# Kernel tuning notes

Measured on AMD Instinct MI355X. Metric: run time of the kernel, lower is better.

## Reference

```python
import jax, jax.numpy as jnp
import numpy as np

N1, N2, E = 256, 128, 4096

def _conv(x, w, b):
    # NCHW conv, 3x3, padding=1 (SAME), then ReLU
    y = jax.lax.conv_general_dilated(x, w, (1, 1), 'SAME',
                                     dimension_numbers=('NCHW', 'OIHW', 'NCHW'))
    return jax.nn.relu(y + b[None, :, None, None])

def _pool(x):
    return jax.lax.reduce_window(x, -jnp.inf, jax.lax.max,
                                 (1, 1, 2, 2), (1, 1, 2, 2), 'VALID')

def _sage(x, src, dst, wl, bl, wr, n):
    # torch_geometric SAGEConv: out = lin_l(mean_j x_src) + lin_r(x), then L2 normalize
    agg = jax.ops.segment_sum(x[src], dst, num_segments=n)
    cnt = jax.ops.segment_sum(jnp.ones((src.shape[0],), x.dtype), dst, num_segments=n)
    agg = agg / jnp.maximum(cnt, 1.0)[:, None]
    out = agg @ wl.T + bl + x @ wr.T
    return out / jnp.maximum(jnp.linalg.norm(out, axis=-1, keepdims=True), 1e-12)

def _diff_pool(x, adj, s):
    # torch_geometric dense_diff_pool
    s = jax.nn.softmax(s, axis=-1)
    out = jnp.einsum('bnc,bnf->bcf', s, x)
    out_adj = jnp.einsum('bnc,bnm,bmd->bcd', s, adj, s)
    link = adj - jnp.einsum('bnc,bmc->bnm', s, s)
    link_loss = jnp.sqrt(jnp.sum(link * link)) / adj.size
    ent_loss = jnp.mean(jnp.sum(-s * jnp.log(s + 1e-15), axis=-1))
    return out, out_adj, link_loss, ent_loss

def setup_inputs() -> dict:
    key = jax.random.key(0)
    ks = jax.random.split(key, 16)
    rn = lambda k, shape, sc: jax.random.normal(k, shape, jnp.float32) * sc
    inp = {}
    inp['inputs'] = jax.random.normal(ks[0], (1, 5, 512, 512), jnp.float32)
    inp['edge_index'] = jax.random.randint(ks[1], (2, E), 0, N1)
    chans = [(5, 32), (32, 64), (64, 128), (128, 256), (256, 256)]
    for i, (ci, co) in enumerate(chans):
        inp[f'w{i+1}'] = rn(ks[2 + i], (co, ci, 3, 3), 1.0 / np.sqrt(ci * 9))
        inp[f'b{i+1}'] = jnp.zeros((co,), jnp.float32)
    sdims = [(256, 128), (256, 128), (128, 2)]
    for i, (ci, co) in enumerate(sdims):
        inp[f'sage{i+1}_wl'] = rn(ks[7 + 2 * i], (co, ci), 1.0 / np.sqrt(ci))
        inp[f'sage{i+1}_bl'] = jnp.zeros((co,), jnp.float32)
        inp[f'sage{i+1}_wr'] = rn(ks[8 + 2 * i], (co, ci), 1.0 / np.sqrt(ci))
    return inp

def reference(inputs, edge_index, w1, b1, w2, b2, w3, b3, w4, b4, w5, b5,
              sage1_wl, sage1_bl, sage1_wr, sage2_wl, sage2_bl, sage2_wr,
              sage3_wl, sage3_bl, sage3_wr):
    x = _pool(_conv(inputs, w1, b1))
    x = _pool(_conv(x, w2, b2))
    x = _pool(_conv(x, w3, b3))
    x = _pool(_conv(x, w4, b4))
    x = _pool(_conv(x, w5, b5))            # [1,256,16,16]
    org = x.reshape(N1, N1)                # [256 nodes, 256 feats]
    src, dst = edge_index[0], edge_index[1]
    x1 = _sage(org, src, dst, sage1_wl, sage1_bl, sage1_wr, N1)
    s1 = _sage(org, src, dst, sage2_wl, sage2_bl, sage2_wr, N1)
    # dense adjacency (scipy coo->dense sums duplicate edges)
    adj1 = jnp.zeros((N1, N1), jnp.float32).at[src, dst].add(1.0)
    xp, adjp, ll1, el1 = _diff_pool(x1[None], adj1[None], s1[None])
    xp = xp.reshape(N2, N2)
    adjp = adjp.reshape(N2, N2)
    # vectorized form of the per-row in-place argmax binarization loop
    row_max = jnp.max(adjp, axis=1, keepdims=True)
    edge_out = jnp.where(adjp == row_max, 1.0, 0.0)
    # dense_to_sparse of the binarized matrix (one max per row, generic case)
    cols = jnp.argmax(adjp, axis=1)
    ei2 = jnp.stack([jnp.arange(N2), cols])  # [2,128] int
    nodes_out = jnp.tanh(_sage(xp, ei2[0], ei2[1], sage3_wl, sage3_bl, sage3_wr, N2))
    adj2 = jnp.zeros((N2, N2), jnp.float32).at[ei2[0], ei2[1]].add(1.0)
    s2 = jnp.ones((1, N2, 1), jnp.float32)  # softmax over size-1 dim -> ones
    x2, _, ll2, el2 = _diff_pool(nodes_out[None], adj2[None], s2)
    return (x2.reshape(-1), ll1 + ll2, el1 + el2, nodes_out, edge_out, ei2)
```

## Files before the change

### kernel.cpp

```cpp
#include <hip/hip_runtime.h>
#include <hip/hip_bf16.h>
#include <math.h>

#define N_EDGES 4096
#define NN1 256
#define NN2 128

typedef short v8s __attribute__((ext_vector_type(8)));
typedef float v4f __attribute__((ext_vector_type(4)));

__device__ inline unsigned short f2b(float f){
  union { __hip_bfloat16 h; unsigned short u; } cv;
  cv.h = __float2bfloat16(f);
  return cv.u;
}

template<int NT>
__device__ inline float block_sum(float v, float* red, int t){
  red[t] = v; __syncthreads();
  #pragma unroll
  for (int st = NT/2; st > 0; st >>= 1){
    if (t < st) red[t] += red[t+st];
    __syncthreads();
  }
  float r = red[0]; __syncthreads();
  return r;
}
template<int NT>
__device__ inline float block_max(float v, float* red, int t){
  red[t] = v; __syncthreads();
  #pragma unroll
  for (int st = NT/2; st > 0; st >>= 1){
    if (t < st) red[t] = fmaxf(red[t], red[t+st]);
    __syncthreads();
  }
  float r = red[0]; __syncthreads();
  return r;
}
template<int NT>
__device__ inline int block_min_int(int v, int* red, int t){
  red[t] = v; __syncthreads();
  #pragma unroll
  for (int st = NT/2; st > 0; st >>= 1){
    if (t < st) red[t] = min(red[t], red[t+st]);
    __syncthreads();
  }
  int r = red[0]; __syncthreads();
  return r;
}

template<int CHUNKS, int COUT, int CIN, int SSLABS, int BSTR, int OUTF32>
__global__ __launch_bounds__(256) void conv_mfma(
    const unsigned short* __restrict__ in, const unsigned short* __restrict__ wb,
    const float* __restrict__ bias, unsigned short* __restrict__ outb,
    float* __restrict__ outf,
    int in_row, int in_slab, int out_row, int out_slab)
{
  constexpr int CG = COUT/32;
  __shared__ unsigned short tileb[SSLABS*2600];
  __shared__ unsigned short wldsb[9*32*40];

  const int cg = blockIdx.x % CG, bx = blockIdx.x / CG, by = blockIdx.y;
  const int tid = threadIdx.x, lane = tid & 63, wv = tid >> 6;
  const int cot = wv >> 1, wp = wv & 1;
  const int ml = lane & 15, g = lane >> 4;

  v4f acc[8];
  #pragma unroll
  for (int t = 0; t < 8; ++t) acc[t] = (v4f){0.f,0.f,0.f,0.f};

  for (int cb = 0; cb < CHUNKS; ++cb){
    if (cb) __syncthreads();
    for (int j = tid; j < SSLABS*324; j += 256){
      int s = j / 324, rem = j - s*324;
      int row = rem / 18, px = rem - row*18;
      int gidx = (cb*SSLABS + s)*in_slab + ((by*16 + row)*in_row + bx*16 + px)*8;
      *(v8s*)&tileb[s*2600 + (row*18+px)*8] = *(const v8s*)&in[gidx];
    }
    for (int j = tid; j < 1152; j += 256){
      int k = j >> 7, rem = j & 127;
      int co = rem >> 2, q = rem & 3;
      int gw = (k*COUT + cg*32 + co)*CIN + cb*32 + q*8;
      *(v8s*)&wldsb[(k*32+co)*40 + q*8] = *(const v8s*)&wb[gw];
    }
    __syncthreads();

    #pragma unroll
    for (int k9 = 0; k9 < 9; ++k9){
      const int ky = k9/3, kx = k9 - 3*(k9/3);
      v8s a = *(const v8s*)&wldsb[(k9*32 + cot*16 + ml)*40 + g*8];
      #pragma unroll
      for (int tt = 0; tt < 8; ++tt){
        int t = wp*8 + tt;
        v8s b = *(const v8s*)&tileb[g*BSTR + ((t+ky)*18 + kx + ml)*8];
        acc[tt] = __builtin_amdgcn_mfma_f32_16x16x32_bf16(a, b, acc[tt], 0, 0, 0);
      }
    }
  }

  const int cob = cg*32 + cot*16 + g*4;
  float b4[4] = {bias[cob], bias[cob+1], bias[cob+2], bias[cob+3]};
  #pragma unroll
  for (int tp = 0; tp < 4; ++tp){
    float m[4];
    #pragma unroll
    for (int r = 0; r < 4; ++r){
      float v = fmaxf(acc[2*tp][r], acc[2*tp+1][r]);
      float o = __shfl_xor(v, 1);
      m[r] = fmaxf(fmaxf(v, o) + b4[r], 0.f);
    }
    if ((lane & 1) == 0){
      int gy = by*8 + wp*4 + tp, gx = bx*8 + (ml >> 1);
      if (OUTF32){
        #pragma unroll
        for (int r = 0; r < 4; ++r)
          outf[(cob + r)*256 + gy*16 + gx] = m[r];
      } else {
        unsigned int u0 = (unsigned)f2b(m[0]) | ((unsigned)f2b(m[1]) << 16);
        unsigned int u1 = (unsigned)f2b(m[2]) | ((unsigned)f2b(m[3]) << 16);
        int slabo = cob >> 3, sub = (g & 1)*4;
        size_t idx = (size_t)slabo*out_slab + (size_t)((gy+1)*out_row + gx+1)*8 + sub;
        *(uint2*)(outb + idx) = make_uint2(u0, u1);
      }
    }
  }
}

__global__ __launch_bounds__(256) void prep_kernel(
    const float* __restrict__ src, unsigned short* __restrict__ p0b,
    const float* __restrict__ w1, const float* __restrict__ w2,
    const float* __restrict__ w3, const float* __restrict__ w4,
    const float* __restrict__ w5, unsigned short* __restrict__ wbb,
    const float* __restrict__ a, const float* __restrict__ b2,
    const float* __restrict__ c2, const float* __restrict__ d2,
    float* __restrict__ o)
{
  int b = blockIdx.x, tid = threadIdx.x;
  if (b < 1024){
    int idx = b*256 + tid;
    int y = idx >> 9, x = idx & 511;
    unsigned short v8[8];
    #pragma unroll
    for (int c = 0; c < 5; ++c) v8[c] = f2b(src[c*262144 + y*512 + x]);
    v8[5] = 0; v8[6] = 0; v8[7] = 0;
    *(uint4*)&p0b[((size_t)(y+1)*516 + (x+1))*8] = *(uint4*)v8;
  } else if (b < 1452){
    int j = (b-1024)*256 + tid;
    int co, ci, CO, CIl, CIsrc, dst; const float* w;
    if (j < 1024)      { co=j>>5;        ci=j&31;        w=w1; CIsrc=5;   CO=32;  CIl=32;  dst=0; }
    else if (j < 3072) { int q=j-1024;   co=q>>5;  ci=q&31;  w=w2; CIsrc=32;  CO=64;  CIl=32;  dst=9216; }
    else if (j < 11264){ int q=j-3072;   co=q>>6;  ci=q&63;  w=w3; CIsrc=64;  CO=128; CIl=64;  dst=27648; }
    else if (j < 44032){ int q=j-11264;  co=q>>7;  ci=q&127; w=w4; CIsrc=128; CO=256; CIl=128; dst=101376; }
    else               { int q=j-44032;  co=q>>8;  ci=q&255; w=w5; CIsrc=256; CO=256; CIl=256; dst=396288; }
    #pragma unroll
    for (int k = 0; k < 9; ++k){
      float val = (ci < CIsrc) ? w[(co*CIsrc + ci)*9 + k] : 0.f;
      wbb[dst + (k*CO + co)*CIl + ci] = f2b(val);
    }
  } else {
    int idx = (b-1452)*256 + tid;
    int m = idx >> 15, rem = idx & 32767, k = rem >> 7, cc = rem & 127;
    const float* sp = (m==0)?a:(m==1)?b2:(m==2)?c2:d2;
    o[m*32768 + k*128 + cc] = sp[cc*256 + k];
  }
}

__global__ void build_adj_kernel(const int* __restrict__ ei, float* adj, float* cnt){
  int e = blockIdx.x*256 + threadIdx.x;
  if (e < N_EDGES){
    int s = ei[e], d = ei[N_EDGES + e];
    atomicAdd(&adj[s*NN1 + d], 1.0f);
    atomicAdd(&cnt[d], 1.0f);
  }
}

__global__ __launch_bounds__(128) void sage12_kernel(
    const float* __restrict__ adj, const float* __restrict__ cnt,
    const float* __restrict__ org,
    const float* __restrict__ wl1t, const float* __restrict__ bl1, const float* __restrict__ wr1t,
    const float* __restrict__ wl2t, const float* __restrict__ bl2, const float* __restrict__ wr2t,
    float* __restrict__ x1, float* __restrict__ s_out, float* __restrict__ st,
    float* __restrict__ entpart)
{
  __shared__ float sa[NN1], so[NN1], col[NN1], red[128];
  int n = blockIdx.x, c = threadIdx.x;
  for (int k = c; k < NN1; k += 128){
    col[k] = adj[k*NN1 + n];
    so[k]  = org[n*NN1 + k];
  }
  __syncthreads();
  float a0 = 0.f, a1 = 0.f;
  #pragma unroll 4
  for (int s2 = 0; s2 < NN1; ++s2){
    float av = col[s2];
    a0 += av * org[s2*NN1 + c];
    a1 += av * org[s2*NN1 + c + 128];
  }
  float cd = fmaxf(cnt[n], 1.0f);
  sa[c] = a0 / cd;
  sa[c+128] = a1 / cd;
  __syncthreads();

  float p1 = bl1[c], p2 = bl2[c];
  for (int k = 0; k < NN1; ++k){
    float av = sa[k], ov = so[k];
    p1 += av*wl1t[k*128+c] + ov*wr1t[k*128+c];
    p2 += av*wl2t[k*128+c] + ov*wr2t[k*128+c];
  }
  float n1s = block_sum<128>(p1*p1, red, c);
  x1[n*128 + c] = p1 / fmaxf(sqrtf(n1s), 1e-12f);
  float n2s = block_sum<128>(p2*p2, red, c);
  float p2n = p2 / fmaxf(sqrtf(n2s), 1e-12f);
  float mx = block_max<128>(p2n, red, c);
  float ev = expf(p2n - mx);
  float ssum = block_sum<128>(ev, red, c);
  float sv = ev / ssum;
  s_out[n*128 + c] = sv;
  st[c*NN1 + n] = sv;
  float esum = block_sum<128>(-sv * logf(sv + 1e-15f), red, c);
  if (c == 0) entpart[n] = esum;
}

__global__ __launch_bounds__(256) void fuse1_kernel(
    const float* __restrict__ s, const float* __restrict__ x1,
    const float* __restrict__ adj, const float* __restrict__ st,
    float* __restrict__ xp, float* __restrict__ t, float* __restrict__ linkpart)
{
  __shared__ float sn[128]; __shared__ float red[256];
  int b = blockIdx.x, tid = threadIdx.x;
  if (b < 64){
    int cc = b*2 + (tid >> 7), f = tid & 127;
    float acc = 0.f;
    for (int n = 0; n < NN1; ++n) acc += s[n*128+cc] * x1[n*128+f];
    xp[cc*128+f] = acc;
  } else if (b < 192){
    int n = (b-64)*2 + (tid >> 7), c = tid & 127;
    float acc = 0.f;
    for (int m = 0; m < NN1; ++m){
      float a = adj[n*NN1+m];
      if (a != 0.f) acc += a * s[m*128+c];
    }
    t[n*128+c] = acc;
  } else {
    int n = b - 192, m = tid;
    if (m < 128) sn[m] = s[n*128+m];
    __syncthreads();
    float dot = 0.f;
    for (int c = 0; c < 128; ++c) dot += sn[c]*st[c*NN1 + m];
    float v = adj[n*NN1+m] - dot;
    float part = block_sum<256>(v*v, red, m);
    if (m == 0) linkpart[n] = part;
  }
}

__global__ __launch_bounds__(128) void adjp_kernel(const float* __restrict__ s,
    const float* __restrict__ t, float* __restrict__ adjp){
  int cc = blockIdx.x, d = threadIdx.x;
  float acc = 0.f;
  for (int n = 0; n < NN1; ++n) acc += s[n*128+cc] * t[n*128+d];
  adjp[cc*128+d] = acc;
}

__global__ __launch_bounds__(128) void binarize_kernel(const float* __restrict__ adjp,
    float* __restrict__ edge_out, float* __restrict__ ei2_out, int* __restrict__ cols){
  __shared__ float red[128]; __shared__ int redi[128];
  int i = blockIdx.x, j = threadIdx.x;
  float v = adjp[i*128+j];
  float mx = block_max<128>(v, red, j);
  edge_out[i*128+j] = (v == mx) ? 1.0f : 0.0f;
  int cand = (v == mx) ? j : (1 << 30);
  int cmin = block_min_int<128>(cand, redi, j);
  if (j == 0){
    cols[i] = cmin;
    ei2_out[i] = (float)i;
    ei2_out[128 + i] = (float)cmin;
  }
}

__global__ __launch_bounds__(128) void sage3_agg_kernel(const float* __restrict__ xp,
    const int* __restrict__ cols, float* __restrict__ aggn3){
  int d = blockIdx.x, f = threadIdx.x;
  float acc = 0.f, c = 0.f;
  for (int i = 0; i < NN2; ++i){
    if (cols[i] == d){ acc += xp[i*128+f]; c += 1.f; }
  }
  aggn3[d*128+f] = acc / fmaxf(c, 1.f);
}

__global__ __launch_bounds__(128) void sage3_out_kernel(const float* __restrict__ aggn3,
    const float* __restrict__ xp,
    const float* __restrict__ wl3, const float* __restrict__ bl3, const float* __restrict__ wr3,
    float* __restrict__ nodes_out)
{
  __shared__ float red[128];
  int n = blockIdx.x, k = threadIdx.x;
  float ag = aggn3[n*128+k];
  float xv = xp[n*128+k];
  float q0 = block_sum<128>(ag*wl3[k]     + xv*wr3[k],     red, k);
  float q1 = block_sum<128>(ag*wl3[128+k] + xv*wr3[128+k], red, k);
  if (k == 0){
    float p0 = q0 + bl3[0], p1 = q1 + bl3[1];
    float nm = fmaxf(sqrtf(p0*p0 + p1*p1), 1e-12f);
    nodes_out[n*2+0] = tanhf(p0/nm);
    nodes_out[n*2+1] = tanhf(p1/nm);
  }
}

__global__ __launch_bounds__(256) void finalize_kernel(const float* __restrict__ linkpart,
    const float* __restrict__ entpart, float* __restrict__ d_out)
{
  __shared__ float red[256];
  int t = threadIdx.x;
  float ls = block_sum<256>(linkpart[t], red, t);
  float es = block_sum<256>(entpart[t], red, t);
  float v0 = 0.f, v1 = 0.f;
  if (t < 128){ v0 = d_out[4 + t*2 + 0]; v1 = d_out[4 + t*2 + 1]; }
  float s0 = block_sum<256>(v0, red, t);
  float s1 = block_sum<256>(v1, red, t);
  if (t == 0){
    d_out[0] = s0;
    d_out[1] = s1;
    d_out[2] = sqrtf(ls)/65536.0f + sqrtf(16256.0f)/16384.0f;
    d_out[3] = es/256.0f;
  }
}

extern "C" void kernel_launch(void* const* d_in, const int* in_sizes, int n_in,
                              void* d_out_v, int out_size, void* d_ws, size_t ws_size,
                              hipStream_t stream)
{
  (void)in_sizes; (void)n_in; (void)out_size; (void)ws_size;
  const float* input = (const float*)d_in[0];
  const int*   ei    = (const int*)  d_in[1];
  const float* w1 = (const float*)d_in[2];  const float* b1 = (const float*)d_in[3];
  const float* w2 = (const float*)d_in[4];  const float* b2 = (const float*)d_in[5];
  const float* w3 = (const float*)d_in[6];  const float* b3 = (const float*)d_in[7];
  const float* w4 = (const float*)d_in[8];  const float* b4 = (const float*)d_in[9];
  const float* w5 = (const float*)d_in[10]; const float* b5 = (const float*)d_in[11];
  const float* s1wl = (const float*)d_in[12]; const float* s1bl = (const float*)d_in[13];
  const float* s1wr = (const float*)d_in[14];
  const float* s2wl = (const float*)d_in[15]; const float* s2bl = (const float*)d_in[16];
  const float* s2wr = (const float*)d_in[17];
  const float* s3wl = (const float*)d_in[18]; const float* s3bl = (const float*)d_in[19];
  const float* s3wr = (const float*)d_in[20];
  float* d_out = (float*)d_out_v;
  float* ws = (float*)d_ws;

  unsigned short* P0b = (unsigned short*)(ws);
  unsigned short* Pb1 = (unsigned short*)(ws + 1060896);
  unsigned short* Pb2 = (unsigned short*)(ws + 2134176);
  unsigned short* Pb3 = (unsigned short*)(ws + 2683296);
  unsigned short* Pb4 = (unsigned short*)(ws + 2970528);
  unsigned short* wb  = (unsigned short*)(ws + 3127200);
  float* org = ws + 3620256;
  float* wt  = ws + 3685792;
  float* st  = ws + 3816864;
  float* G   = ws + 3849632;

  float* adj1     = G;
  float* cnt      = G + 65536;
  float* aggn3    = G + 65792;
  float* x1       = G + 147712;
  float* s        = G + 180480;
  float* t        = G + 213248;
  float* xp       = G + 246016;
  float* adjp     = G + 262400;
  int*   cols     = (int*)(G + 278784);
  float* linkpart = G + 278912;
  float* entpart  = G + 279168;

  hipMemsetAsync(ws, 0, (size_t)3127200*sizeof(float), stream);
  prep_kernel<<<dim3(1964), 256, 0, stream>>>(input, P0b, w1, w2, w3, w4, w5, wb,
                                              s1wl, s1wr, s2wl, s2wr, wt);

  conv_mfma<1,32,32,1,0,0>      <<<dim3(32,32), 256, 0, stream>>>(P0b, wb,        b1, Pb1, nullptr, 516, 2121792, 260, 536640);
  conv_mfma<1,64,32,4,2600,0>   <<<dim3(32,16), 256, 0, stream>>>(Pb1, wb+9216,   b2, Pb2, nullptr, 260, 536640, 132, 137280);
  conv_mfma<2,128,64,4,2600,0>  <<<dim3(32,8),  256, 0, stream>>>(Pb2, wb+27648,  b3, Pb3, nullptr, 132, 137280, 68,  35904);
  conv_mfma<4,256,128,4,2600,0> <<<dim3(32,4),  256, 0, stream>>>(Pb3, wb+101376, b4, Pb4, nullptr, 68,  35904,  36,  9792);
  conv_mfma<8,256,256,4,2600,1> <<<dim3(16,2),  256, 0, stream>>>(Pb4, wb+396288, b5, nullptr, org, 36,  9792,   0,   0);

  hipMemsetAsync(adj1, 0, (65536 + 256)*sizeof(float), stream);
  build_adj_kernel<<<dim3(16),  256, 0, stream>>>(ei, adj1, cnt);
  sage12_kernel   <<<dim3(256), 128, 0, stream>>>(adj1, cnt, org, wt, s1bl, wt+32768,
                                                  wt+65536, s2bl, wt+98304, x1, s, st, entpart);
  fuse1_kernel    <<<dim3(448), 256, 0, stream>>>(s, x1, adj1, st, xp, t, linkpart);
  adjp_kernel     <<<dim3(128), 128, 0, stream>>>(s, t, adjp);
  binarize_kernel <<<dim3(128), 128, 0, stream>>>(adjp, d_out + 260, d_out + 16644, cols);
  sage3_agg_kernel<<<dim3(128), 128, 0, stream>>>(xp, cols, aggn3);
  sage3_out_kernel<<<dim3(128), 128, 0, stream>>>(aggn3, xp, s3wl, s3bl, s3wr, d_out + 4);
  finalize_kernel <<<dim3(1),   256, 0, stream>>>(linkpart, entpart, d_out);
}
```

Before: 220.6 us.

## Zero only padded halos and fuse adjp/binarize and sage3 kernels

Replaces the large workspace memset (about 12.5 MB) with a small kernel that zeroes only the one-pixel halo borders of each padded bf16 activation buffer plus the adjacency and count arrays. It also fuses the adjp matmul with the row-argmax binarization, and the sage3 aggregation with its output projection, cutting two launches and two intermediate buffers. This removes a large memory-fill cost and launch overhead. It relies on the conv kernels fully overwriting the buffer interiors, so any interior not written would now hold stale data.

```diff
diff --git a/kernel.cpp b/kernel.cpp
--- a/kernel.cpp
+++ b/kernel.cpp
@@ -124,6 +124,30 @@
       }
     }
   }
+}
+
+__global__ __launch_bounds__(256) void zero_kernel(unsigned short* __restrict__ wsb,
+                                                   float* __restrict__ adjz)
+{
+  int j = blockIdx.x*256 + threadIdx.x;
+  const int c0=2056, c1=6184, c2=10344, c3=14568, c4=18920, ca=35368;
+  if (j >= ca) return;
+  if (j >= c4){
+    int q = j - c4;
+    ((float4*)adjz)[q] = make_float4(0.f,0.f,0.f,0.f);
+    return;
+  }
+  int base, P, R, W, per, rem;
+  if (j < c0)      { base=0;       P=516; R=514; W=512; per=2056; rem=j; }
+  else if (j < c1) { base=2121792; P=260; R=258; W=256; per=1032; rem=j-c0; }
+  else if (j < c2) { base=4268352; P=132; R=130; W=128; per=520;  rem=j-c1; }
+  else if (j < c3) { base=5366592; P=68;  R=66;  W=64;  per=264;  rem=j-c2; }
+  else             { base=5941056; P=36;  R=34;  W=32;  per=136;  rem=j-c3; }
+  int s = rem / per, r2 = rem - s*per;
+  int row, px;
+  if (r2 < 2*P){ row = (r2 < P) ? 0 : R-1; px = (r2 < P) ? r2 : r2 - P; }
+  else { int q = r2 - 2*P; row = 1 + (q >> 1); px = (q & 1) ? (W+1) : 0; }
+  *(uint4*)&wsb[(size_t)base + ((size_t)(s*R + row)*P + px)*8] = make_uint4(0,0,0,0);
 }
 
 __global__ __launch_bounds__(256) void prep_kernel(
@@ -253,52 +277,46 @@
   }
 }
 
-__global__ __launch_bounds__(128) void adjp_kernel(const float* __restrict__ s,
-    const float* __restrict__ t, float* __restrict__ adjp){
-  int cc = blockIdx.x, d = threadIdx.x;
+__global__ __launch_bounds__(128) void adjp_bin_kernel(
+    const float* __restrict__ s, const float* __restrict__ t,
+    float* __restrict__ edge_out, float* __restrict__ ei2_out, int* __restrict__ cols)
+{
+  __shared__ float scol[NN1]; __shared__ float red[128]; __shared__ int redi[128];
+  int cc = blockIdx.x, j = threadIdx.x;
+  scol[j]       = s[j*128 + cc];
+  scol[j + 128] = s[(j+128)*128 + cc];
+  __syncthreads();
   float acc = 0.f;
-  for (int n = 0; n < NN1; ++n) acc += s[n*128+cc] * t[n*128+d];
-  adjp[cc*128+d] = acc;
-}
-
-__global__ __launch_bounds__(128) void binarize_kernel(const float* __restrict__ adjp,
-    float* __restrict__ edge_out, float* __restrict__ ei2_out, int* __restrict__ cols){
-  __shared__ float red[128]; __shared__ int redi[128];
-  int i = blockIdx.x, j = threadIdx.x;
-  float v = adjp[i*128+j];
-  float mx = block_max<128>(v, red, j);
-  edge_out[i*128+j] = (v == mx) ? 1.0f : 0.0f;
-  int cand = (v == mx) ? j : (1 << 30);
+  for (int n = 0; n < NN1; ++n) acc += scol[n] * t[n*128 + j];
+  float mx = block_max<128>(acc, red, j);
+  edge_out[cc*128+j] = (acc == mx) ? 1.0f : 0.0f;
+  int cand = (acc == mx) ? j : (1 << 30);
   int cmin = block_min_int<128>(cand, redi, j);
   if (j == 0){
-    cols[i] = cmin;
-    ei2_out[i] = (float)i;
-    ei2_out[128 + i] = (float)cmin;
-  }
-}
-
-__global__ __launch_bounds__(128) void sage3_agg_kernel(const float* __restrict__ xp,
-    const int* __restrict__ cols, float* __restrict__ aggn3){
-  int d = blockIdx.x, f = threadIdx.x;
+    cols[cc] = cmin;
+    ei2_out[cc] = (float)cc;
+    ei2_out[128 + cc] = (float)cmin;
+  }
+}
+
+__global__ __launch_bounds__(128) void sage3_kernel(
+    const float* __restrict__ xp, const int* __restrict__ cols,
+    const float* __restrict__ wl3, const float* __restrict__ bl3,
+    const float* __restrict__ wr3, float* __restrict__ nodes_out)
+{
+  __shared__ int colsl[NN2]; __shared__ float red[128];
+  int n = blockIdx.x, f = threadIdx.x;
+  colsl[f] = cols[f];
+  __syncthreads();
   float acc = 0.f, c = 0.f;
   for (int i = 0; i < NN2; ++i){
-    if (cols[i] == d){ acc += xp[i*128+f]; c += 1.f; }
-  }
-  aggn3[d*128+f] = acc / fmaxf(c, 1.f);
-}
-
-__global__ __launch_bounds__(128) void sage3_out_kernel(const float* __restrict__ aggn3,
-    const float* __restrict__ xp,
-    const float* __restrict__ wl3, const float* __restrict__ bl3, const float* __restrict__ wr3,
-    float* __restrict__ nodes_out)
-{
-  __shared__ float red[128];
-  int n = blockIdx.x, k = threadIdx.x;
-  float ag = aggn3[n*128+k];
-  float xv = xp[n*128+k];
-  float q0 = block_sum<128>(ag*wl3[k]     + xv*wr3[k],     red, k);
-  float q1 = block_sum<128>(ag*wl3[128+k] + xv*wr3[128+k], red, k);
-  if (k == 0){
+    if (colsl[i] == n){ acc += xp[i*128+f]; c += 1.f; }
+  }
+  float ag = acc / fmaxf(c, 1.f);
+  float xv = xp[n*128+f];
+  float q0 = block_sum<128>(ag*wl3[f]     + xv*wr3[f],     red, f);
+  float q1 = block_sum<128>(ag*wl3[128+f] + xv*wr3[128+f], red, f);
+  if (f == 0){
     float p0 = q0 + bl3[0], p1 = q1 + bl3[1];
     float nm = fmaxf(sqrtf(p0*p0 + p1*p1), 1e-12f);
     nodes_out[n*2+0] = tanhf(p0/nm);
@@ -359,17 +377,15 @@
 
   float* adj1     = G;
   float* cnt      = G + 65536;
-  float* aggn3    = G + 65792;
   float* x1       = G + 147712;
   float* s        = G + 180480;
   float* t        = G + 213248;
   float* xp       = G + 246016;
-  float* adjp     = G + 262400;
   int*   cols     = (int*)(G + 278784);
   float* linkpart = G + 278912;
   float* entpart  = G + 279168;
 
-  hipMemsetAsync(ws, 0, (size_t)3127200*sizeof(float), stream);
+  zero_kernel<<<dim3(139), 256, 0, stream>>>((unsigned short*)ws, adj1);
   prep_kernel<<<dim3(1964), 256, 0, stream>>>(input, P0b, w1, w2, w3, w4, w5, wb,
                                               s1wl, s1wr, s2wl, s2wr, wt);
 
@@ -379,14 +395,11 @@
   conv_mfma<4,256,128,4,2600,0> <<<dim3(32,4),  256, 0, stream>>>(Pb3, wb+101376, b4, Pb4, nullptr, 68,  35904,  36,  9792);
   conv_mfma<8,256,256,4,2600,1> <<<dim3(16,2),  256, 0, stream>>>(Pb4, wb+396288, b5, nullptr, org, 36,  9792,   0,   0);
 
-  hipMemsetAsync(adj1, 0, (65536 + 256)*sizeof(float), stream);
   build_adj_kernel<<<dim3(16),  256, 0, stream>>>(ei, adj1, cnt);
   sage12_kernel   <<<dim3(256), 128, 0, stream>>>(adj1, cnt, org, wt, s1bl, wt+32768,
                                                   wt+65536, s2bl, wt+98304, x1, s, st, entpart);
   fuse1_kernel    <<<dim3(448), 256, 0, stream>>>(s, x1, adj1, st, xp, t, linkpart);
-  adjp_kernel     <<<dim3(128), 128, 0, stream>>>(s, t, adjp);
-  binarize_kernel <<<dim3(128), 128, 0, stream>>>(adjp, d_out + 260, d_out + 16644, cols);
-  sage3_agg_kernel<<<dim3(128), 128, 0, stream>>>(xp, cols, aggn3);
-  sage3_out_kernel<<<dim3(128), 128, 0, stream>>>(aggn3, xp, s3wl, s3bl, s3wr, d_out + 4);
+  adjp_bin_kernel <<<dim3(128), 128, 0, stream>>>(s, t, d_out + 260, d_out + 16644, cols);
+  sage3_kernel    <<<dim3(128), 128, 0, stream>>>(xp, cols, s3wl, s3bl, s3wr, d_out + 4);
   finalize_kernel <<<dim3(1),   256, 0, stream>>>(linkpart, entpart, d_out);
 }
```

After: 209.9 us. -4.9%, faster.
